# Performance work log

Measured on AMD Instinct MI355X. Metric: run time of the kernel, lower is better.

Reference implementation:

```python
import jax, jax.numpy as jnp
import numpy as np

B = 256        # graphs
NODES = 116    # nodes per view per graph
FEAT = 115     # node feature dim
LENN = 6670    # edges per view per graph (116*115/2)
SEG2 = 13456   # raw edges per graph in input (2*LENN + 116 discarded)
HID = 128      # hidden_channels
HC = 512       # hc


def setup_inputs() -> dict:
    key = jax.random.key(0)
    ks = jax.random.split(key, 12)
    x = jax.random.normal(ks[0], (B * 2 * NODES, FEAT), jnp.float32)
    # per-graph edge layout: [6670 FC edges | 6670 SC edges | 116 dummy]
    off = (2 * NODES) * jnp.arange(B, dtype=jnp.int32)  # [B]
    fc = jax.random.randint(ks[1], (2, B, LENN), 0, NODES, dtype=jnp.int32) + off[None, :, None]
    sc = jax.random.randint(ks[2], (2, B, LENN), 0, NODES, dtype=jnp.int32) + off[None, :, None] + NODES
    dummy = jnp.zeros((2, B, SEG2 - 2 * LENN), jnp.int32) + off[None, :, None]
    edge_index = jnp.concatenate([fc, sc, dummy], axis=2).reshape(2, B * SEG2)
    edge_weight = jax.random.uniform(ks[3], (B * SEG2,), jnp.float32)
    batch = jnp.repeat(jnp.arange(B, dtype=jnp.int32), 2 * NODES)
    s = 1.0 / np.sqrt(FEAT)
    W1 = jax.random.uniform(ks[4], (FEAT, HID), jnp.float32, -s, s)
    b1 = jnp.zeros((HID,), jnp.float32)
    W2 = jax.random.uniform(ks[5], (FEAT, HID), jnp.float32, -s, s)
    b2 = jnp.zeros((HID,), jnp.float32)
    s6 = 1.0 / np.sqrt(2 * NODES)
    W6 = jax.random.uniform(ks[6], (2 * NODES, HC), jnp.float32, -s6, s6)
    b6 = jax.random.uniform(ks[7], (HC,), jnp.float32, -s6, s6)
    s7 = 1.0 / np.sqrt(HC)
    W7 = jax.random.uniform(ks[8], (HC, 1), jnp.float32, -s7, s7)
    b7 = jax.random.uniform(ks[9], (1,), jnp.float32, -s7, s7)
    return dict(x=x, edge_index=edge_index, edge_weight=edge_weight, batch=batch,
                W1=W1, b1=b1, W2=W2, b2=b2, W6=W6, b6=b6, W7=W7, b7=b7)


def _gcn_conv(x, ei, ew, W, b, num_nodes):
    """PyG GCNConv: D^-1/2 (A+I) D^-1/2 X W + b (self-loop weight 1)."""
    h = x @ W                                   # [N, HID]
    src, dst = ei[0], ei[1]
    deg = jax.ops.segment_sum(ew, dst, num_segments=num_nodes) + 1.0  # +1 self-loop
    dinv = jax.lax.rsqrt(deg)                   # [N]
    norm = dinv[src] * ew * dinv[dst]           # [E]
    out = jax.ops.segment_sum(h[src] * norm[:, None], dst, num_segments=num_nodes)
    out = out + (dinv * dinv)[:, None] * h      # self-loop message
    return out + b


def reference(x, edge_index, edge_weight, batch, W1, b1, W2, b2, W6, b6, W7, b7):
    gidx = jnp.arange(B, dtype=edge_index.dtype)
    ei = edge_index.reshape(2, B, SEG2)
    ew = edge_weight.reshape(B, SEG2)
    # de-offset per-graph edges into per-view node index spaces (116 nodes/graph)
    ei_fc = (ei[:, :, :LENN] - NODES * gidx[None, :, None]).reshape(2, B * LENN)
    ei_sc = (ei[:, :, LENN:2 * LENN] - NODES * (gidx + 1)[None, :, None]).reshape(2, B * LENN)
    ew_fc = ew[:, :LENN].reshape(-1)
    ew_sc = ew[:, LENN:2 * LENN].reshape(-1)
    xr = x.reshape(B, 2 * NODES, FEAT)
    node_fc = xr[:, :NODES].reshape(B * NODES, FEAT)
    node_sc = xr[:, NODES:].reshape(B * NODES, FEAT)
    N = B * NODES
    x1 = _gcn_conv(node_fc, ei_fc, ew_fc, W1, b1, N).max(axis=1)  # [B*116]
    x2 = _gcn_conv(node_sc, ei_sc, ew_sc, W2, b2, N).max(axis=1)  # [B*116]
    feat = jnp.stack([x1, x2], axis=1).reshape(B, 2 * NODES)      # flatten()
    # dropout p=0.5 is identity in eval mode
    h = jax.nn.relu(feat @ W6 + b6)
    return h @ W7 + b7  # [B, 1]
```

## Files before the change

kernel.cpp:

```cpp
#include <hip/hip_runtime.h>


#define NB 256
#define NODES 116
#define FEAT 115
#define LENN 6670
#define SEG2 13456
#define HID 128
#define HC 512

typedef float f32x4 __attribute__((ext_vector_type(4)));
typedef short short8 __attribute__((ext_vector_type(8)));
typedef __bf16 bf16x8 __attribute__((ext_vector_type(8)));

#define MFMA16(a, b, c) __builtin_amdgcn_mfma_f32_16x16x32_bf16( \
    __builtin_bit_cast(bf16x8, (a)), __builtin_bit_cast(bf16x8, (b)), (c), 0, 0, 0)

#define OFF_ALO 32768
#define OFF_BHI 65536
#define OFF_BLO 98304
#define OFF_PMAX 131072
#define OFF_DINV 133120
#define LDS_BYTES 133632

__device__ __forceinline__ unsigned f2bf(float f) {
  unsigned u = __builtin_bit_cast(unsigned, f);
  return (u + 0x7FFFu + ((u >> 16) & 1u)) >> 16;
}
__device__ __forceinline__ float bf2f(unsigned h) {
  return __builtin_bit_cast(float, h << 16);
}
__device__ __forceinline__ int kperm(int k) {
  return (k & ~31) | (k & 3) | (((k >> 2) & 3) << 3) | (((k >> 4) & 1) << 2);
}
__device__ __forceinline__ int swzb(int row, int kbyte) {
  return row * 256 + (kbyte ^ ((row & 7) << 4));
}
__device__ __forceinline__ f32x4 splat4(float f) {
  f32x4 r = {f, f, f, f};
  return r;
}

__global__ __launch_bounds__(1024, 1) void k_fused(
    const float* __restrict__ x, const int* __restrict__ ei,
    const float* __restrict__ ew,
    const float* __restrict__ W1, const float* __restrict__ b1,
    const float* __restrict__ W2, const float* __restrict__ b2,
    float* __restrict__ featws)
{
  __shared__ __align__(16) char sm[LDS_BYTES];
  float* Af = (float*)sm;
  float* dinv = (float*)(sm + OFF_DINV);
  float* pmaxp = (float*)(sm + OFF_PMAX);
  const int bid = blockIdx.x;
  const int g = bid >> 1, v = bid & 1;
  const int tid = threadIdx.x;

  {
    f32x4 z = splat4(0.f);
    f32x4* p = (f32x4*)sm;
#pragma unroll
    for (int i = 0; i < 8; ++i) p[tid + (i << 10)] = z;
  }
  __syncthreads();

  const int eoff = g * SEG2 + v * LENN;
  const int nbase = g * 232 + v * 116;
  {
    const int* __restrict__ srcp = ei + eoff;
    const int* __restrict__ dstp = ei + (size_t)NB * SEG2 + eoff;
    const float* __restrict__ wp = ew + eoff;
    for (int q = tid; q < (LENN / 2); q += 1024) {
      int2 s2 = ((const int2*)srcp)[q];
      int2 d2 = ((const int2*)dstp)[q];
      float2 w2 = ((const float2*)wp)[q];
      atomicAdd(&Af[((d2.x - nbase) << 7) + (s2.x - nbase)], w2.x);
      atomicAdd(&Af[((d2.y - nbase) << 7) + (s2.y - nbase)], w2.y);
    }
    const float* __restrict__ xg = x + (size_t)nbase * FEAT;
    for (int idx = tid; idx < NODES * FEAT; idx += 1024) {
      int s = idx / FEAT;
      int c = idx - s * FEAT;
      float f = xg[idx];
      unsigned hi = f2bf(f);
      unsigned lo = f2bf(f - bf2f(hi));
      int byte = swzb(c, kperm(s) << 1);
      *(unsigned short*)(sm + OFF_BHI + byte) = (unsigned short)hi;
      *(unsigned short*)(sm + OFF_BLO + byte) = (unsigned short)lo;
    }
  }
  __syncthreads();

  if (tid < 4 * NODES) {
    const int r = tid >> 2, q = tid & 3;
    const float* row = Af + (r << 7) + q * 29;
    float s = 0.f;
#pragma unroll
    for (int j = 0; j < 29; ++j) s += row[j];
    s += __shfl_xor(s, 1, 64);
    s += __shfl_xor(s, 2, 64);
    if (q == 0) dinv[r] = rsqrtf(s + 1.0f);
  }
  __syncthreads();

  for (int idx = tid; idx < NODES * 128; idx += 1024) {
    int d = idx >> 7, s = idx & 127;
    if (s < NODES) {
      float di = dinv[d];
      float val = Af[idx] * (di * dinv[s]);
      if (d == s) val += di * di;
      Af[idx] = val;
    }
  }
  __syncthreads();

  {
    const int t16 = tid << 4;
    const int row = t16 >> 7;
    const int k0 = t16 & 127;
    f32x4 vv[4];
#pragma unroll
    for (int q2 = 0; q2 < 4; ++q2) vv[q2] = *(f32x4*)(Af + t16 + (q2 << 2));
    __syncthreads();
#pragma unroll
    for (int q2 = 0; q2 < 4; ++q2)
#pragma unroll
      for (int j = 0; j < 4; ++j) {
        float f = vv[q2][j];
        unsigned hi = f2bf(f);
        unsigned lo = f2bf(f - bf2f(hi));
        int byte = swzb(row, kperm(k0 + (q2 << 2) + j) << 1);
        *(unsigned short*)(sm + byte) = (unsigned short)hi;
        *(unsigned short*)(sm + OFF_ALO + byte) = (unsigned short)lo;
      }
  }
  __syncthreads();

  const int lane = tid & 63, w = tid >> 6;
  const int mg = w >> 2, ng = w & 3;
  const int rA0 = (mg << 5) + (lane & 15), rA1 = rA0 + 16;
  const int rB0 = (ng << 5) + (lane & 15), rB1 = rB0 + 16;
  const int kb = (lane >> 4) << 4;

  f32x4 acc00 = splat4(0.f), acc01 = splat4(0.f);
  f32x4 acc10 = splat4(0.f), acc11 = splat4(0.f);

#pragma unroll
  for (int kc = 0; kc < 4; ++kc) {
    const int ko = (kc << 6) + kb;
    short8 a0h = *(const short8*)(sm + swzb(rA0, ko));
    short8 a0l = *(const short8*)(sm + OFF_ALO + swzb(rA0, ko));
    short8 a1h = *(const short8*)(sm + swzb(rA1, ko));
    short8 a1l = *(const short8*)(sm + OFF_ALO + swzb(rA1, ko));
    short8 b0h = *(const short8*)(sm + OFF_BHI + swzb(rB0, ko));
    short8 b0l = *(const short8*)(sm + OFF_BLO + swzb(rB0, ko));
    short8 b1h = *(const short8*)(sm + OFF_BHI + swzb(rB1, ko));
    short8 b1l = *(const short8*)(sm + OFF_BLO + swzb(rB1, ko));
    acc00 = MFMA16(a0h, b0h, acc00); acc00 = MFMA16(a0l, b0h, acc00); acc00 = MFMA16(a0h, b0l, acc00);
    acc01 = MFMA16(a0h, b1h, acc01); acc01 = MFMA16(a0l, b1h, acc01); acc01 = MFMA16(a0h, b1l, acc01);
    acc10 = MFMA16(a1h, b0h, acc10); acc10 = MFMA16(a1l, b0h, acc10); acc10 = MFMA16(a1h, b0l, acc10);
    acc11 = MFMA16(a1h, b1h, acc11); acc11 = MFMA16(a1l, b1h, acc11); acc11 = MFMA16(a1h, b1l, acc11);
  }
  __syncthreads();

  {
#pragma unroll
    for (int mt = 0; mt < 2; ++mt)
#pragma unroll
      for (int nt = 0; nt < 2; ++nt)
#pragma unroll
        for (int r2 = 0; r2 < 4; ++r2) {
          f32x4 a = (mt == 0) ? (nt == 0 ? acc00 : acc01)
                              : (nt == 0 ? acc10 : acc11);
          float f = a[r2];
          int row = (mg << 5) + (mt << 4) + ((lane >> 4) << 2) + r2;
          int col = (ng << 5) + (nt << 4) + (lane & 15);
          unsigned hi = f2bf(f);
          unsigned lo = f2bf(f - bf2f(hi));
          int byte = swzb(row, kperm(col) << 1);
          *(unsigned short*)(sm + byte) = (unsigned short)hi;
          *(unsigned short*)(sm + OFF_ALO + byte) = (unsigned short)lo;
        }
    const float* __restrict__ Wv = v ? W2 : W1;
    for (int idx = tid; idx < FEAT * HID; idx += 1024) {
      int k = idx >> 7, c = idx & 127;
      float f = Wv[idx];
      unsigned hi = f2bf(f);
      unsigned lo = f2bf(f - bf2f(hi));
      int byte = swzb(c, kperm(k) << 1);
      *(unsigned short*)(sm + OFF_BHI + byte) = (unsigned short)hi;
      *(unsigned short*)(sm + OFF_BLO + byte) = (unsigned short)lo;
    }
  }
  __syncthreads();

  {
    const float* __restrict__ bv = v ? b2 : b1;
    float bb0 = bv[(ng << 5) + (lane & 15)];
    float bb1 = bv[(ng << 5) + 16 + (lane & 15)];
    acc00 = splat4(bb0); acc01 = splat4(bb1);
    acc10 = splat4(bb0); acc11 = splat4(bb1);
  }
#pragma unroll
  for (int kc = 0; kc < 4; ++kc) {
    const int ko = (kc << 6) + kb;
    short8 a0h = *(const short8*)(sm + swzb(rA0, ko));
    short8 a0l = *(const short8*)(sm + OFF_ALO + swzb(rA0, ko));
    short8 a1h = *(const short8*)(sm + swzb(rA1, ko));
    short8 a1l = *(const short8*)(sm + OFF_ALO + swzb(rA1, ko));
    short8 b0h = *(const short8*)(sm + OFF_BHI + swzb(rB0, ko));
    short8 b0l = *(const short8*)(sm + OFF_BLO + swzb(rB0, ko));
    short8 b1h = *(const short8*)(sm + OFF_BHI + swzb(rB1, ko));
    short8 b1l = *(const short8*)(sm + OFF_BLO + swzb(rB1, ko));
    acc00 = MFMA16(a0h, b0h, acc00); acc00 = MFMA16(a0l, b0h, acc00); acc00 = MFMA16(a0h, b0l, acc00);
    acc01 = MFMA16(a0h, b1h, acc01); acc01 = MFMA16(a0l, b1h, acc01); acc01 = MFMA16(a0h, b1l, acc01);
    acc10 = MFMA16(a1h, b0h, acc10); acc10 = MFMA16(a1l, b0h, acc10); acc10 = MFMA16(a1h, b0l, acc10);
    acc11 = MFMA16(a1h, b1h, acc11); acc11 = MFMA16(a1l, b1h, acc11); acc11 = MFMA16(a1h, b1l, acc11);
  }

#pragma unroll
  for (int mt = 0; mt < 2; ++mt)
#pragma unroll
    for (int r2 = 0; r2 < 4; ++r2) {
      f32x4 aN0 = (mt == 0) ? acc00 : acc10;
      f32x4 aN1 = (mt == 0) ? acc01 : acc11;
      float m = fmaxf(aN0[r2], aN1[r2]);
      m = fmaxf(m, __shfl_xor(m, 1, 64));
      m = fmaxf(m, __shfl_xor(m, 2, 64));
      m = fmaxf(m, __shfl_xor(m, 4, 64));
      m = fmaxf(m, __shfl_xor(m, 8, 64));
      if ((lane & 15) == 0) {
        int row = (mg << 5) + (mt << 4) + ((lane >> 4) << 2) + r2;
        pmaxp[(ng << 7) + row] = m;
      }
    }
  __syncthreads();
  if (tid < NODES) {
    float m = fmaxf(fmaxf(pmaxp[tid], pmaxp[128 + tid]),
                    fmaxf(pmaxp[256 + tid], pmaxp[384 + tid]));
    featws[g * 232 + 2 * tid + v] = m;
  }
}

__global__ __launch_bounds__(1024) void k_mlp(
    const float* __restrict__ featws, const float* __restrict__ W6,
    const float* __restrict__ b6, const float* __restrict__ W7,
    const float* __restrict__ b7, float* __restrict__ out)
{
  __shared__ float sf[232];
  __shared__ float ph[512];
  __shared__ float red[8];
  const int g = blockIdx.x, tid = threadIdx.x;
  if (tid < 232) sf[tid] = featws[g * 232 + tid];
  __syncthreads();

  const int col = tid & 511, half = tid >> 9;
  const float* __restrict__ w6p = W6 + (size_t)(half * 116) * HC + col;
  const float* __restrict__ sfh = sf + half * 116;
  float p = 0.f;
#pragma unroll 4
  for (int k = 0; k < 116; ++k)
    p = fmaf(sfh[k], w6p[(size_t)k * HC], p);
  if (half) ph[col] = p;
  __syncthreads();

  if (!half) {
    float a = b6[col] + p + ph[col];
    a = fmaxf(a, 0.f) * W7[col];
#pragma unroll
    for (int off = 32; off >= 1; off >>= 1) a += __shfl_xor(a, off, 64);
    if ((tid & 63) == 0) red[tid >> 6] = a;
  }
  __syncthreads();
  if (tid == 0) {
    float t = b7[0];
#pragma unroll
    for (int i = 0; i < 8; ++i) t += red[i];
    out[g] = t;
  }
}

extern "C" void kernel_launch(void* const* d_in, const int* in_sizes, int n_in,
                              void* d_out, int out_size, void* d_ws, size_t ws_size,
                              hipStream_t stream)
{
  const float* x  = (const float*)d_in[0];
  const int*   ei = (const int*)d_in[1];
  const float* ew = (const float*)d_in[2];
  const float* W1 = (const float*)d_in[4];
  const float* b1 = (const float*)d_in[5];
  const float* W2 = (const float*)d_in[6];
  const float* b2 = (const float*)d_in[7];
  const float* W6 = (const float*)d_in[8];
  const float* b6 = (const float*)d_in[9];
  const float* W7 = (const float*)d_in[10];
  const float* b7 = (const float*)d_in[11];

  float* featws = (float*)d_ws;
  float* out    = (float*)d_out;

  hipLaunchKernelGGL(k_fused, dim3(2 * NB), dim3(1024), 0, stream,
                     x, ei, ew, W1, b1, W2, b2, featws);
  hipLaunchKernelGGL(k_mlp,   dim3(NB),     dim3(1024), 0, stream,
                     featws, W6, b6, W7, b7, out);
}
```

Before: 182.2 us.

## Fuse both GCN views and MLP head into one kernel per graph

Merges the per-view GCN kernel and the MLP kernel into a single kernel with one block per graph that loops over both views, then runs the MLP head from LDS-resident features. This removes the second launch and the global workspace round trip. It also pads the dense adjacency rows to a stride of 117 to spread LDS atomics across banks, and packs bf16 hi/lo split conversions two at a time into 32-bit stores. In exchange the grid shrinks from 512 to 256 blocks, so the two views run serially within a block and fewer CUs are busy.

```diff
diff --git a/kernel.cpp b/kernel.cpp
--- a/kernel.cpp
+++ b/kernel.cpp
@@ -8,6 +8,7 @@
 #define SEG2 13456
 #define HID 128
 #define HC 512
+#define AF_STR 117
 
 typedef float f32x4 __attribute__((ext_vector_type(4)));
 typedef short short8 __attribute__((ext_vector_type(8)));
@@ -21,7 +22,9 @@
 #define OFF_BLO 98304
 #define OFF_PMAX 131072
 #define OFF_DINV 133120
-#define LDS_BYTES 133632
+#define OFF_FEAT 133632
+#define OFF_RED  134560
+#define LDS_BYTES 134592
 
 __device__ __forceinline__ unsigned f2bf(float f) {
   unsigned u = __builtin_bit_cast(unsigned, f);
@@ -30,6 +33,11 @@
 __device__ __forceinline__ float bf2f(unsigned h) {
   return __builtin_bit_cast(float, h << 16);
 }
+__device__ __forceinline__ void cvt2(float v0, float v1, unsigned& hi, unsigned& lo) {
+  unsigned h0 = f2bf(v0), h1 = f2bf(v1);
+  hi = h0 | (h1 << 16);
+  lo = f2bf(v0 - bf2f(h0)) | (f2bf(v1 - bf2f(h1)) << 16);
+}
 __device__ __forceinline__ int kperm(int k) {
   return (k & ~31) | (k & 3) | (((k >> 2) & 3) << 3) | (((k >> 4) & 1) << 2);
 }
@@ -41,242 +49,239 @@
   return r;
 }
 
-__global__ __launch_bounds__(1024, 1) void k_fused(
+__global__ __launch_bounds__(1024, 1) void k_all(
     const float* __restrict__ x, const int* __restrict__ ei,
     const float* __restrict__ ew,
     const float* __restrict__ W1, const float* __restrict__ b1,
     const float* __restrict__ W2, const float* __restrict__ b2,
-    float* __restrict__ featws)
+    const float* __restrict__ W6, const float* __restrict__ b6,
+    const float* __restrict__ W7, const float* __restrict__ b7,
+    float* __restrict__ out)
 {
   __shared__ __align__(16) char sm[LDS_BYTES];
-  float* Af = (float*)sm;
-  float* dinv = (float*)(sm + OFF_DINV);
+  float* Af    = (float*)sm;
+  float* dinv  = (float*)(sm + OFF_DINV);
   float* pmaxp = (float*)(sm + OFF_PMAX);
-  const int bid = blockIdx.x;
-  const int g = bid >> 1, v = bid & 1;
+  float* sfeat = (float*)(sm + OFF_FEAT);
+  float* redp  = (float*)(sm + OFF_RED);
+  const int g = blockIdx.x;
   const int tid = threadIdx.x;
-
-  {
-    f32x4 z = splat4(0.f);
-    f32x4* p = (f32x4*)sm;
-#pragma unroll
-    for (int i = 0; i < 8; ++i) p[tid + (i << 10)] = z;
-  }
-  __syncthreads();
-
-  const int eoff = g * SEG2 + v * LENN;
-  const int nbase = g * 232 + v * 116;
-  {
-    const int* __restrict__ srcp = ei + eoff;
-    const int* __restrict__ dstp = ei + (size_t)NB * SEG2 + eoff;
-    const float* __restrict__ wp = ew + eoff;
-    for (int q = tid; q < (LENN / 2); q += 1024) {
-      int2 s2 = ((const int2*)srcp)[q];
-      int2 d2 = ((const int2*)dstp)[q];
-      float2 w2 = ((const float2*)wp)[q];
-      atomicAdd(&Af[((d2.x - nbase) << 7) + (s2.x - nbase)], w2.x);
-      atomicAdd(&Af[((d2.y - nbase) << 7) + (s2.y - nbase)], w2.y);
-    }
-    const float* __restrict__ xg = x + (size_t)nbase * FEAT;
-    for (int idx = tid; idx < NODES * FEAT; idx += 1024) {
-      int s = idx / FEAT;
-      int c = idx - s * FEAT;
-      float f = xg[idx];
-      unsigned hi = f2bf(f);
-      unsigned lo = f2bf(f - bf2f(hi));
-      int byte = swzb(c, kperm(s) << 1);
-      *(unsigned short*)(sm + OFF_BHI + byte) = (unsigned short)hi;
-      *(unsigned short*)(sm + OFF_BLO + byte) = (unsigned short)lo;
-    }
-  }
-  __syncthreads();
-
-  if (tid < 4 * NODES) {
-    const int r = tid >> 2, q = tid & 3;
-    const float* row = Af + (r << 7) + q * 29;
-    float s = 0.f;
-#pragma unroll
-    for (int j = 0; j < 29; ++j) s += row[j];
-    s += __shfl_xor(s, 1, 64);
-    s += __shfl_xor(s, 2, 64);
-    if (q == 0) dinv[r] = rsqrtf(s + 1.0f);
-  }
-  __syncthreads();
-
-  for (int idx = tid; idx < NODES * 128; idx += 1024) {
-    int d = idx >> 7, s = idx & 127;
-    if (s < NODES) {
-      float di = dinv[d];
-      float val = Af[idx] * (di * dinv[s]);
-      if (d == s) val += di * di;
-      Af[idx] = val;
-    }
-  }
-  __syncthreads();
-
-  {
-    const int t16 = tid << 4;
-    const int row = t16 >> 7;
-    const int k0 = t16 & 127;
-    f32x4 vv[4];
-#pragma unroll
-    for (int q2 = 0; q2 < 4; ++q2) vv[q2] = *(f32x4*)(Af + t16 + (q2 << 2));
-    __syncthreads();
-#pragma unroll
-    for (int q2 = 0; q2 < 4; ++q2)
-#pragma unroll
-      for (int j = 0; j < 4; ++j) {
-        float f = vv[q2][j];
-        unsigned hi = f2bf(f);
-        unsigned lo = f2bf(f - bf2f(hi));
-        int byte = swzb(row, kperm(k0 + (q2 << 2) + j) << 1);
-        *(unsigned short*)(sm + byte) = (unsigned short)hi;
-        *(unsigned short*)(sm + OFF_ALO + byte) = (unsigned short)lo;
-      }
-  }
-  __syncthreads();
-
   const int lane = tid & 63, w = tid >> 6;
   const int mg = w >> 2, ng = w & 3;
   const int rA0 = (mg << 5) + (lane & 15), rA1 = rA0 + 16;
   const int rB0 = (ng << 5) + (lane & 15), rB1 = rB0 + 16;
   const int kb = (lane >> 4) << 4;
-
-  f32x4 acc00 = splat4(0.f), acc01 = splat4(0.f);
-  f32x4 acc10 = splat4(0.f), acc11 = splat4(0.f);
-
-#pragma unroll
-  for (int kc = 0; kc < 4; ++kc) {
-    const int ko = (kc << 6) + kb;
-    short8 a0h = *(const short8*)(sm + swzb(rA0, ko));
-    short8 a0l = *(const short8*)(sm + OFF_ALO + swzb(rA0, ko));
-    short8 a1h = *(const short8*)(sm + swzb(rA1, ko));
-    short8 a1l = *(const short8*)(sm + OFF_ALO + swzb(rA1, ko));
-    short8 b0h = *(const short8*)(sm + OFF_BHI + swzb(rB0, ko));
-    short8 b0l = *(const short8*)(sm + OFF_BLO + swzb(rB0, ko));
-    short8 b1h = *(const short8*)(sm + OFF_BHI + swzb(rB1, ko));
-    short8 b1l = *(const short8*)(sm + OFF_BLO + swzb(rB1, ko));
-    acc00 = MFMA16(a0h, b0h, acc00); acc00 = MFMA16(a0l, b0h, acc00); acc00 = MFMA16(a0h, b0l, acc00);
-    acc01 = MFMA16(a0h, b1h, acc01); acc01 = MFMA16(a0l, b1h, acc01); acc01 = MFMA16(a0h, b1l, acc01);
-    acc10 = MFMA16(a1h, b0h, acc10); acc10 = MFMA16(a1l, b0h, acc10); acc10 = MFMA16(a1h, b0l, acc10);
-    acc11 = MFMA16(a1h, b1h, acc11); acc11 = MFMA16(a1l, b1h, acc11); acc11 = MFMA16(a1h, b1l, acc11);
+  const int arow = tid >> 3, aseg = tid & 7;
+
+  for (int v = 0; v < 2; ++v) {
+    {
+      f32x4 z = splat4(0.f);
+      f32x4* p = (f32x4*)sm;
+      for (int i = tid; i < 3393; i += 1024) p[i] = z;
+    }
+    __syncthreads();
+
+    const int eoff = g * SEG2 + v * LENN;
+    const int nbase = g * 232 + v * 116;
+
+    {
+      const int* __restrict__ srcp = ei + eoff;
+      const int* __restrict__ dstp = ei + (size_t)NB * SEG2 + eoff;
+      const float* __restrict__ wp = ew + eoff;
+      for (int q = tid; q < (LENN / 2); q += 1024) {
+        int2 s2 = ((const int2*)srcp)[q];
+        int2 d2 = ((const int2*)dstp)[q];
+        float2 w2 = ((const float2*)wp)[q];
+        atomicAdd(&Af[(d2.x - nbase) * AF_STR + (s2.x - nbase)], w2.x);
+        atomicAdd(&Af[(d2.y - nbase) * AF_STR + (s2.y - nbase)], w2.y);
+      }
+      const float* __restrict__ xg = x + (size_t)nbase * FEAT;
+#pragma unroll
+      for (int i = 0; i < 8; ++i) {
+        int unit = tid + (i << 10);
+        int sp = unit >> 7, c = unit & 127;
+        int s0 = sp << 1, s1 = s0 + 1;
+        float x0 = (c < FEAT && s0 < NODES) ? xg[s0 * FEAT + c] : 0.f;
+        float x1 = (c < FEAT && s1 < NODES) ? xg[s1 * FEAT + c] : 0.f;
+        unsigned hi, lo;
+        cvt2(x0, x1, hi, lo);
+        int byte = swzb(c, kperm(s0) << 1);
+        *(unsigned*)(sm + OFF_BHI + byte) = hi;
+        *(unsigned*)(sm + OFF_BLO + byte) = lo;
+      }
+    }
+    __syncthreads();
+
+    if (tid < 4 * NODES) {
+      const int r = tid >> 2, q = tid & 3;
+      const float* row = Af + r * AF_STR + q * 29;
+      float s = 0.f;
+#pragma unroll
+      for (int j = 0; j < 29; ++j) s += row[j];
+      s += __shfl_xor(s, 1, 64);
+      s += __shfl_xor(s, 2, 64);
+      if (q == 0) dinv[r] = rsqrtf(s + 1.0f);
+    }
+    __syncthreads();
+
+    float av[16];
+    if (arow < NODES) {
+      float dr = dinv[arow];
+#pragma unroll
+      for (int j = 0; j < 16; ++j) {
+        int c = (aseg << 4) + j;
+        float t = 0.f;
+        if (c < NODES) {
+          t = Af[arow * AF_STR + c] * (dr * dinv[c]);
+          if (c == arow) t += dr * dr;
+        }
+        av[j] = t;
+      }
+    }
+    __syncthreads();
+
+    if (arow < NODES) {
+#pragma unroll
+      for (int jp = 0; jp < 8; ++jp) {
+        int c = (aseg << 4) + (jp << 1);
+        unsigned hi, lo;
+        cvt2(av[2 * jp], av[2 * jp + 1], hi, lo);
+        int byte = swzb(arow, kperm(c) << 1);
+        *(unsigned*)(sm + byte) = hi;
+        *(unsigned*)(sm + OFF_ALO + byte) = lo;
+      }
+    }
+    __syncthreads();
+
+    f32x4 acc00 = splat4(0.f), acc01 = splat4(0.f);
+    f32x4 acc10 = splat4(0.f), acc11 = splat4(0.f);
+#pragma unroll
+    for (int kc = 0; kc < 4; ++kc) {
+      const int ko = (kc << 6) + kb;
+      short8 a0h = *(const short8*)(sm + swzb(rA0, ko));
+      short8 a0l = *(const short8*)(sm + OFF_ALO + swzb(rA0, ko));
+      short8 a1h = *(const short8*)(sm + swzb(rA1, ko));
+      short8 a1l = *(const short8*)(sm + OFF_ALO + swzb(rA1, ko));
+      short8 b0h = *(const short8*)(sm + OFF_BHI + swzb(rB0, ko));
+      short8 b0l = *(const short8*)(sm + OFF_BLO + swzb(rB0, ko));
+      short8 b1h = *(const short8*)(sm + OFF_BHI + swzb(rB1, ko));
+      short8 b1l = *(const short8*)(sm + OFF_BLO + swzb(rB1, ko));
+      acc00 = MFMA16(a0h, b0h, acc00); acc00 = MFMA16(a0l, b0h, acc00); acc00 = MFMA16(a0h, b0l, acc00);
+      acc01 = MFMA16(a0h, b1h, acc01); acc01 = MFMA16(a0l, b1h, acc01); acc01 = MFMA16(a0h, b1l, acc01);
+      acc10 = MFMA16(a1h, b0h, acc10); acc10 = MFMA16(a1l, b0h, acc10); acc10 = MFMA16(a1h, b0l, acc10);
+      acc11 = MFMA16(a1h, b1h, acc11); acc11 = MFMA16(a1l, b1h, acc11); acc11 = MFMA16(a1h, b1l, acc11);
+    }
+    __syncthreads();
+
+    {
+#pragma unroll
+      for (int mt = 0; mt < 2; ++mt)
+#pragma unroll
+        for (int nt = 0; nt < 2; ++nt)
+#pragma unroll
+          for (int r2 = 0; r2 < 4; ++r2) {
+            f32x4 a = (mt == 0) ? (nt == 0 ? acc00 : acc01)
+                                : (nt == 0 ? acc10 : acc11);
+            float f = a[r2];
+            int row = (mg << 5) + (mt << 4) + ((lane >> 4) << 2) + r2;
+            int col = (ng << 5) + (nt << 4) + (lane & 15);
+            unsigned hi = f2bf(f);
+            unsigned lo = f2bf(f - bf2f(hi));
+            int byte = swzb(row, kperm(col) << 1);
+            *(unsigned short*)(sm + byte) = (unsigned short)hi;
+            *(unsigned short*)(sm + OFF_ALO + byte) = (unsigned short)lo;
+          }
+      const float* __restrict__ Wv = v ? W2 : W1;
+#pragma unroll
+      for (int i = 0; i < 8; ++i) {
+        int unit = tid + (i << 10);
+        int kp = unit >> 7, c = unit & 127;
+        int k0 = kp << 1, k1 = k0 + 1;
+        float w0 = (k0 < FEAT) ? Wv[(size_t)k0 * HID + c] : 0.f;
+        float w1 = (k1 < FEAT) ? Wv[(size_t)k1 * HID + c] : 0.f;
+        unsigned hi, lo;
+        cvt2(w0, w1, hi, lo);
+        int byte = swzb(c, kperm(k0) << 1);
+        *(unsigned*)(sm + OFF_BHI + byte) = hi;
+        *(unsigned*)(sm + OFF_BLO + byte) = lo;
+      }
+    }
+    __syncthreads();
+
+    {
+      const float* __restrict__ bv = v ? b2 : b1;
+      float bb0 = bv[(ng << 5) + (lane & 15)];
+      float bb1 = bv[(ng << 5) + 16 + (lane & 15)];
+      acc00 = splat4(bb0); acc01 = splat4(bb1);
+      acc10 = splat4(bb0); acc11 = splat4(bb1);
+    }
+#pragma unroll
+    for (int kc = 0; kc < 4; ++kc) {
+      const int ko = (kc << 6) + kb;
+      short8 a0h = *(const short8*)(sm + swzb(rA0, ko));
+      short8 a0l = *(const short8*)(sm + OFF_ALO + swzb(rA0, ko));
+      short8 a1h = *(const short8*)(sm + swzb(rA1, ko));
+      short8 a1l = *(const short8*)(sm + OFF_ALO + swzb(rA1, ko));
+      short8 b0h = *(const short8*)(sm + OFF_BHI + swzb(rB0, ko));
+      short8 b0l = *(const short8*)(sm + OFF_BLO + swzb(rB0, ko));
+      short8 b1h = *(const short8*)(sm + OFF_BHI + swzb(rB1, ko));
+      short8 b1l = *(const short8*)(sm + OFF_BLO + swzb(rB1, ko));
+      acc00 = MFMA16(a0h, b0h, acc00); acc00 = MFMA16(a0l, b0h, acc00); acc00 = MFMA16(a0h, b0l, acc00);
+      acc01 = MFMA16(a0h, b1h, acc01); acc01 = MFMA16(a0l, b1h, acc01); acc01 = MFMA16(a0h, b1l, acc01);
+      acc10 = MFMA16(a1h, b0h, acc10); acc10 = MFMA16(a1l, b0h, acc10); acc10 = MFMA16(a1h, b0l, acc10);
+      acc11 = MFMA16(a1h, b1h, acc11); acc11 = MFMA16(a1l, b1h, acc11); acc11 = MFMA16(a1h, b1l, acc11);
+    }
+
+#pragma unroll
+    for (int mt = 0; mt < 2; ++mt)
+#pragma unroll
+      for (int r2 = 0; r2 < 4; ++r2) {
+        f32x4 aN0 = (mt == 0) ? acc00 : acc10;
+        f32x4 aN1 = (mt == 0) ? acc01 : acc11;
+        float m = fmaxf(aN0[r2], aN1[r2]);
+        m = fmaxf(m, __shfl_xor(m, 1, 64));
+        m = fmaxf(m, __shfl_xor(m, 2, 64));
+        m = fmaxf(m, __shfl_xor(m, 4, 64));
+        m = fmaxf(m, __shfl_xor(m, 8, 64));
+        if ((lane & 15) == 0) {
+          int row = (mg << 5) + (mt << 4) + ((lane >> 4) << 2) + r2;
+          pmaxp[(ng << 7) + row] = m;
+        }
+      }
+    __syncthreads();
+    if (tid < NODES) {
+      float m = fmaxf(fmaxf(pmaxp[tid], pmaxp[128 + tid]),
+                      fmaxf(pmaxp[256 + tid], pmaxp[384 + tid]));
+      sfeat[2 * tid + v] = m;
+    }
+    __syncthreads();
   }
-  __syncthreads();
 
   {
-#pragma unroll
-    for (int mt = 0; mt < 2; ++mt)
-#pragma unroll
-      for (int nt = 0; nt < 2; ++nt)
-#pragma unroll
-        for (int r2 = 0; r2 < 4; ++r2) {
-          f32x4 a = (mt == 0) ? (nt == 0 ? acc00 : acc01)
-                              : (nt == 0 ? acc10 : acc11);
-          float f = a[r2];
-          int row = (mg << 5) + (mt << 4) + ((lane >> 4) << 2) + r2;
-          int col = (ng << 5) + (nt << 4) + (lane & 15);
-          unsigned hi = f2bf(f);
-          unsigned lo = f2bf(f - bf2f(hi));
-          int byte = swzb(row, kperm(col) << 1);
-          *(unsigned short*)(sm + byte) = (unsigned short)hi;
-          *(unsigned short*)(sm + OFF_ALO + byte) = (unsigned short)lo;
-        }
-    const float* __restrict__ Wv = v ? W2 : W1;
-    for (int idx = tid; idx < FEAT * HID; idx += 1024) {
-      int k = idx >> 7, c = idx & 127;
-      float f = Wv[idx];
-      unsigned hi = f2bf(f);
-      unsigned lo = f2bf(f - bf2f(hi));
-      int byte = swzb(c, kperm(k) << 1);
-      *(unsigned short*)(sm + OFF_BHI + byte) = (unsigned short)hi;
-      *(unsigned short*)(sm + OFF_BLO + byte) = (unsigned short)lo;
-    }
-  }
-  __syncthreads();
-
-  {
-    const float* __restrict__ bv = v ? b2 : b1;
-    float bb0 = bv[(ng << 5) + (lane & 15)];
-    float bb1 = bv[(ng << 5) + 16 + (lane & 15)];
-    acc00 = splat4(bb0); acc01 = splat4(bb1);
-    acc10 = splat4(bb0); acc11 = splat4(bb1);
-  }
-#pragma unroll
-  for (int kc = 0; kc < 4; ++kc) {
-    const int ko = (kc << 6) + kb;
-    short8 a0h = *(const short8*)(sm + swzb(rA0, ko));
-    short8 a0l = *(const short8*)(sm + OFF_ALO + swzb(rA0, ko));
-    short8 a1h = *(const short8*)(sm + swzb(rA1, ko));
-    short8 a1l = *(const short8*)(sm + OFF_ALO + swzb(rA1, ko));
-    short8 b0h = *(const short8*)(sm + OFF_BHI + swzb(rB0, ko));
-    short8 b0l = *(const short8*)(sm + OFF_BLO + swzb(rB0, ko));
-    short8 b1h = *(const short8*)(sm + OFF_BHI + swzb(rB1, ko));
-    short8 b1l = *(const short8*)(sm + OFF_BLO + swzb(rB1, ko));
-    acc00 = MFMA16(a0h, b0h, acc00); acc00 = MFMA16(a0l, b0h, acc00); acc00 = MFMA16(a0h, b0l, acc00);
-    acc01 = MFMA16(a0h, b1h, acc01); acc01 = MFMA16(a0l, b1h, acc01); acc01 = MFMA16(a0h, b1l, acc01);
-    acc10 = MFMA16(a1h, b0h, acc10); acc10 = MFMA16(a1l, b0h, acc10); acc10 = MFMA16(a1h, b0l, acc10);
-    acc11 = MFMA16(a1h, b1h, acc11); acc11 = MFMA16(a1l, b1h, acc11); acc11 = MFMA16(a1h, b1l, acc11);
-  }
-
-#pragma unroll
-  for (int mt = 0; mt < 2; ++mt)
-#pragma unroll
-    for (int r2 = 0; r2 < 4; ++r2) {
-      f32x4 aN0 = (mt == 0) ? acc00 : acc10;
-      f32x4 aN1 = (mt == 0) ? acc01 : acc11;
-      float m = fmaxf(aN0[r2], aN1[r2]);
-      m = fmaxf(m, __shfl_xor(m, 1, 64));
-      m = fmaxf(m, __shfl_xor(m, 2, 64));
-      m = fmaxf(m, __shfl_xor(m, 4, 64));
-      m = fmaxf(m, __shfl_xor(m, 8, 64));
-      if ((lane & 15) == 0) {
-        int row = (mg << 5) + (mt << 4) + ((lane >> 4) << 2) + r2;
-        pmaxp[(ng << 7) + row] = m;
-      }
-    }
-  __syncthreads();
-  if (tid < NODES) {
-    float m = fmaxf(fmaxf(pmaxp[tid], pmaxp[128 + tid]),
-                    fmaxf(pmaxp[256 + tid], pmaxp[384 + tid]));
-    featws[g * 232 + 2 * tid + v] = m;
-  }
-}
-
-__global__ __launch_bounds__(1024) void k_mlp(
-    const float* __restrict__ featws, const float* __restrict__ W6,
-    const float* __restrict__ b6, const float* __restrict__ W7,
-    const float* __restrict__ b7, float* __restrict__ out)
-{
-  __shared__ float sf[232];
-  __shared__ float ph[512];
-  __shared__ float red[8];
-  const int g = blockIdx.x, tid = threadIdx.x;
-  if (tid < 232) sf[tid] = featws[g * 232 + tid];
-  __syncthreads();
-
-  const int col = tid & 511, half = tid >> 9;
-  const float* __restrict__ w6p = W6 + (size_t)(half * 116) * HC + col;
-  const float* __restrict__ sfh = sf + half * 116;
-  float p = 0.f;
+    const int col = tid & 511, half = tid >> 9;
+    const float* __restrict__ w6p = W6 + (size_t)(half * 116) * HC + col;
+    const float* __restrict__ sfh = sfeat + half * 116;
+    float p = 0.f;
 #pragma unroll 4
-  for (int k = 0; k < 116; ++k)
-    p = fmaf(sfh[k], w6p[(size_t)k * HC], p);
-  if (half) ph[col] = p;
-  __syncthreads();
-
-  if (!half) {
-    float a = b6[col] + p + ph[col];
-    a = fmaxf(a, 0.f) * W7[col];
-#pragma unroll
-    for (int off = 32; off >= 1; off >>= 1) a += __shfl_xor(a, off, 64);
-    if ((tid & 63) == 0) red[tid >> 6] = a;
-  }
-  __syncthreads();
-  if (tid == 0) {
-    float t = b7[0];
-#pragma unroll
-    for (int i = 0; i < 8; ++i) t += red[i];
-    out[g] = t;
+    for (int k = 0; k < 116; ++k)
+      p = fmaf(sfh[k], w6p[(size_t)k * HC], p);
+    float* ph = pmaxp;
+    if (half) ph[col] = p;
+    __syncthreads();
+    if (!half) {
+      float a = b6[col] + p + ph[col];
+      a = fmaxf(a, 0.f) * W7[col];
+#pragma unroll
+      for (int off = 32; off >= 1; off >>= 1) a += __shfl_xor(a, off, 64);
+      if ((tid & 63) == 0) redp[tid >> 6] = a;
+    }
+    __syncthreads();
+    if (tid == 0) {
+      float t = b7[0];
+#pragma unroll
+      for (int i = 0; i < 8; ++i) t += redp[i];
+      out[g] = t;
+    }
   }
 }
 
@@ -295,12 +300,8 @@
   const float* b6 = (const float*)d_in[9];
   const float* W7 = (const float*)d_in[10];
   const float* b7 = (const float*)d_in[11];
-
-  float* featws = (float*)d_ws;
-  float* out    = (float*)d_out;
-
-  hipLaunchKernelGGL(k_fused, dim3(2 * NB), dim3(1024), 0, stream,
-                     x, ei, ew, W1, b1, W2, b2, featws);
-  hipLaunchKernelGGL(k_mlp,   dim3(NB),     dim3(1024), 0, stream,
-                     featws, W6, b6, W7, b7, out);
-}
+  float* out = (float*)d_out;
+
+  hipLaunchKernelGGL(k_all, dim3(NB), dim3(1024), 0, stream,
+                     x, ei, ew, W1, b1, W2, b2, W6, b6, W7, b7, out);
+}
```

New measurement: 478.8 us. 163% more time.
